# Kernel tuning notes

Hardware: AMD Instinct MI355X
Metric: run time of the kernel (lower is better)

## Reference

```python
import jax, jax.numpy as jnp
import numpy as np

N, M, K, C, OUT = 200000, 50000, 16, 64, 128
EPS = 1e-5  # torch BatchNorm1d default eps


def _bn(h, gamma, beta, mean, var):
    # BatchNorm1d in eval mode (running statistics)
    return (h - mean) * jax.lax.rsqrt(var + EPS) * gamma + beta


def setup_inputs() -> dict:
    key = jax.random.key(0)
    ks = jax.random.split(key, 8)
    p = jax.random.normal(ks[0], (N, 3), jnp.float32)
    x = jax.random.normal(ks[1], (N, C), jnp.float32)
    idx = jax.random.randint(ks[2], (M,), 0, N)          # FPS-sampled center indices
    knn_idx = jax.random.randint(ks[3], (M, K), 0, N)    # KNN neighbor indices
    # channel_shrinker: Linear(3+C, C, bias=False) -> BN -> ReLU -> Linear(C, 1)
    W1 = jax.random.normal(ks[4], (3 + C, C), jnp.float32) * 0.05  # stored [in,out]
    g1 = jnp.ones((C,), jnp.float32); b1 = jnp.zeros((C,), jnp.float32)
    m1 = jnp.zeros((C,), jnp.float32); v1 = jnp.ones((C,), jnp.float32)
    W2 = jax.random.normal(ks[5], (C, 1), jnp.float32) * 0.05
    b2 = jnp.zeros((1,), jnp.float32)
    # linear2: Linear(C, OUT, bias=False) -> BN -> ReLU
    Wl = jax.random.normal(ks[6], (C, OUT), jnp.float32) * 0.05
    gl = jnp.ones((OUT,), jnp.float32); bl = jnp.zeros((OUT,), jnp.float32)
    ml = jnp.zeros((OUT,), jnp.float32); vl = jnp.ones((OUT,), jnp.float32)
    return {"p": p, "x": x, "W1": W1, "g1": g1, "b1": b1, "m1": m1, "v1": v1,
            "W2": W2, "b2": b2, "Wl": Wl, "gl": gl, "bl": bl, "ml": ml, "vl": vl,
            "idx": idx, "knn_idx": knn_idx}


def reference(p, x, W1, g1, b1, m1, v1, W2, b2, Wl, gl, bl, ml, vl, idx, knn_idx):
    # queryandgroup(use_xyz=True): relative xyz of neighbors + gathered features
    n_p = p[idx]                                   # [M,3] sampled centers
    rel = p[knn_idx] - n_p[:, None, :]             # [M,K,3]
    x_knn = jnp.concatenate([rel, x[knn_idx]], -1) # [M,K,3+C]
    # channel_shrinker
    h = jnp.maximum(_bn(x_knn @ W1, g1, b1, m1, v1), 0.0)   # [M,K,C]
    s = h @ W2 + b2                                          # [M,K,1]
    prob = jax.nn.softmax(s, axis=1)                         # softmax over neighbors
    # linear2 on ALL original points, then gather by knn_idx
    y = jnp.maximum(_bn(x @ Wl, gl, bl, ml, vl), 0.0)        # [N,OUT]
    y_knn = y[knn_idx]                                       # [M,K,OUT]
    out = jnp.sum(y_knn * prob, axis=1)                      # [M,OUT]
    return n_p, out
```

## Files before the change

### kernel.cpp

```cpp
#include <hip/hip_runtime.h>

#define EPS 1e-5f

typedef __attribute__((ext_vector_type(8))) short bf16x8;
typedef __attribute__((ext_vector_type(4))) float f32x4;

static __device__ __forceinline__ unsigned short f2bf(float f) {
  unsigned int u = __float_as_uint(f);
  u = u + 0x7FFFu + ((u >> 16) & 1u);
  return (unsigned short)(u >> 16);
}
static __device__ __forceinline__ float bf2f(unsigned short h) {
  return __uint_as_float(((unsigned int)h) << 16);
}
static __device__ __forceinline__ unsigned int pk2(float lo, float hi) {
  return (unsigned int)f2bf(lo) | ((unsigned int)f2bf(hi) << 16);
}

__global__ __launch_bounds__(256) void k1_mfma(
    const float* __restrict__ x, const float* __restrict__ W1,
    const float* __restrict__ Wl, const float* __restrict__ gl,
    const float* __restrict__ bl, const float* __restrict__ ml,
    const float* __restrict__ vl,
    unsigned short* __restrict__ Z, unsigned short* __restrict__ Y)
{
  __shared__ unsigned short As[64 * 64];
  __shared__ unsigned short Bs[192 * 64];
  char* Ab = reinterpret_cast<char*>(As);
  char* Bb = reinterpret_cast<char*>(Bs);

  const int t = threadIdx.x;
  const long row0 = (long)blockIdx.x * 64;

  {
    int k = t >> 2, c0 = (t & 3) * 16;
    const float4* w4 = reinterpret_cast<const float4*>(W1 + (size_t)(3 + k) * 64 + c0);
#pragma unroll
    for (int i = 0; i < 4; ++i) {
      float4 w = w4[i];
#pragma unroll
      for (int j = 0; j < 4; ++j) {
        int c = c0 + i * 4 + j;
        float v = (j == 0) ? w.x : (j == 1) ? w.y : (j == 2) ? w.z : w.w;
        int byte = c * 128 + ((2 * k) ^ ((c & 7) << 4));
        *reinterpret_cast<unsigned short*>(Bb + byte) = f2bf(v);
      }
    }
  }
  {
    int k = t >> 2, c0 = (t & 3) * 32;
    const float4* w4 = reinterpret_cast<const float4*>(Wl + (size_t)k * 128 + c0);
#pragma unroll
    for (int i = 0; i < 8; ++i) {
      float4 w = w4[i];
#pragma unroll
      for (int j = 0; j < 4; ++j) {
        int c = 64 + c0 + i * 4 + j;
        float v = (j == 0) ? w.x : (j == 1) ? w.y : (j == 2) ? w.z : w.w;
        int byte = c * 128 + ((2 * k) ^ ((c & 7) << 4));
        *reinterpret_cast<unsigned short*>(Bb + byte) = f2bf(v);
      }
    }
  }
  {
    const float4* xg = reinterpret_cast<const float4*>(x + row0 * 64);
#pragma unroll
    for (int i = 0; i < 4; ++i) {
      int idx = t + i * 256;
      float4 v = xg[idx];
      int r = idx >> 4;
      int b0 = (idx & 15) * 8;
      int byte = r * 128 + (b0 ^ ((r & 7) << 4));
      uint2 pkv = make_uint2(pk2(v.x, v.y), pk2(v.z, v.w));
      *reinterpret_cast<uint2*>(Ab + byte) = pkv;
    }
  }
  __syncthreads();

  const int wid = t >> 6, lane = t & 63;
  const int roff = (wid & 1) * 32, coff = (wid >> 1) * 96;
  const int lr = lane & 15, lk = lane >> 4;

  bf16x8 af[2][2];
#pragma unroll
  for (int rt = 0; rt < 2; ++rt) {
    int r = roff + rt * 16 + lr;
#pragma unroll
    for (int ks = 0; ks < 2; ++ks) {
      int byte = r * 128 + ((ks * 64 + lk * 16) ^ ((r & 7) << 4));
      af[rt][ks] = *reinterpret_cast<const bf16x8*>(Ab + byte);
    }
  }

#pragma unroll
  for (int ct = 0; ct < 6; ++ct) {
    int c0t = coff + ct * 16;
    int cread = c0t + lr;
    int byte0 = cread * 128 + ((lk * 16) ^ ((cread & 7) << 4));
    int byte1 = cread * 128 + ((64 + lk * 16) ^ ((cread & 7) << 4));
    bf16x8 bf0 = *reinterpret_cast<const bf16x8*>(Bb + byte0);
    bf16x8 bf1 = *reinterpret_cast<const bf16x8*>(Bb + byte1);

    float sc0 = 1.f, sc1 = 1.f, sc2 = 1.f, sc3 = 1.f;
    float sh0 = 0.f, sh1 = 0.f, sh2 = 0.f, sh3 = 0.f;
    if (c0t >= 64) {
      int oc = c0t - 64 + lk * 4;
      float4 g4 = *reinterpret_cast<const float4*>(gl + oc);
      float4 v4 = *reinterpret_cast<const float4*>(vl + oc);
      float4 b4 = *reinterpret_cast<const float4*>(bl + oc);
      float4 m4 = *reinterpret_cast<const float4*>(ml + oc);
      sc0 = g4.x * rsqrtf(v4.x + EPS); sh0 = b4.x - m4.x * sc0;
      sc1 = g4.y * rsqrtf(v4.y + EPS); sh1 = b4.y - m4.y * sc1;
      sc2 = g4.z * rsqrtf(v4.z + EPS); sh2 = b4.z - m4.z * sc2;
      sc3 = g4.w * rsqrtf(v4.w + EPS); sh3 = b4.w - m4.w * sc3;
    }
#pragma unroll
    for (int rt = 0; rt < 2; ++rt) {
      f32x4 acc = {0.f, 0.f, 0.f, 0.f};
      acc = __builtin_amdgcn_mfma_f32_16x16x32_bf16(bf0, af[rt][0], acc, 0, 0, 0);
      acc = __builtin_amdgcn_mfma_f32_16x16x32_bf16(bf1, af[rt][1], acc, 0, 0, 0);
      long n = row0 + roff + rt * 16 + lr;
      if (c0t < 64) {
        int cb = c0t + lk * 4;
        *reinterpret_cast<ushort4*>(Z + n * 64 + cb) =
            make_ushort4(f2bf(acc[0]), f2bf(acc[1]), f2bf(acc[2]), f2bf(acc[3]));
      } else {
        int cb = c0t - 64 + lk * 4;
        float y0 = fmaxf(fmaf(acc[0], sc0, sh0), 0.f);
        float y1 = fmaxf(fmaf(acc[1], sc1, sh1), 0.f);
        float y2 = fmaxf(fmaf(acc[2], sc2, sh2), 0.f);
        float y3 = fmaxf(fmaf(acc[3], sc3, sh3), 0.f);
        *reinterpret_cast<ushort4*>(Y + n * 128 + cb) =
            make_ushort4(f2bf(y0), f2bf(y1), f2bf(y2), f2bf(y3));
      }
    }
  }
}

static __device__ __forceinline__ float comb(float a, float b, int off, int lane) {
  bool hi = (lane & off) != 0;
  float send = hi ? a : b;
  float t = __shfl_xor(send, off, 64);
  return (hi ? b : a) + t;
}

__global__ __launch_bounds__(256) void k2_gather(
    const float* __restrict__ p, const unsigned short* __restrict__ Z,
    const unsigned short* __restrict__ Y, const float* __restrict__ W1,
    const float* __restrict__ g1, const float* __restrict__ b1,
    const float* __restrict__ m1, const float* __restrict__ v1,
    const float* __restrict__ W2, const int* __restrict__ idx,
    const int* __restrict__ knn, float* __restrict__ out_np,
    float* __restrict__ out_feat, int M)
{
  int gtid = blockIdx.x * 256 + threadIdx.x;
  int wid = gtid >> 6;
  int lane = threadIdx.x & 63;
  if (wid >= M) return;
  int m = __builtin_amdgcn_readfirstlane(wid);

  float a1 = g1[lane] * rsqrtf(v1[lane] + EPS);
  float c1 = b1[lane] - m1[lane] * a1;
  float w2 = W2[lane];
  float w10 = W1[lane];
  float w11 = W1[64 + lane];
  float w12 = W1[128 + lane];

  int ic = idx[m];
  float cx = p[ic * 3 + 0];
  float cy = p[ic * 3 + 1];
  float cz = p[ic * 3 + 2];
  if (lane < 3) {
    float v = (lane == 0) ? cx : ((lane == 1) ? cy : cz);
    out_np[(size_t)m * 3 + lane] = v;
  }

  float part[16];
  int jj[16];
#pragma unroll
  for (int k = 0; k < 16; ++k) {
    int j = knn[m * 16 + k];
    jj[k] = j;
    float rx = p[j * 3 + 0] - cx;
    float ry = p[j * 3 + 1] - cy;
    float rz = p[j * 3 + 2] - cz;
    float tv = bf2f(Z[(size_t)j * 64 + lane]);
    tv = fmaf(rx, w10, tv);
    tv = fmaf(ry, w11, tv);
    tv = fmaf(rz, w12, tv);
    float h = fmaxf(fmaf(tv, a1, c1), 0.f);
    part[k] = h * w2;
  }

  float u[8];
#pragma unroll
  for (int i = 0; i < 8; ++i) u[i] = comb(part[2 * i], part[2 * i + 1], 32, lane);
  float v4[4];
#pragma unroll
  for (int i = 0; i < 4; ++i) v4[i] = comb(u[2 * i], u[2 * i + 1], 16, lane);
  float w4[2];
#pragma unroll
  for (int i = 0; i < 2; ++i) w4[i] = comb(v4[2 * i], v4[2 * i + 1], 8, lane);
  float s1 = comb(w4[0], w4[1], 4, lane);
  s1 += __shfl_xor(s1, 1, 64);
  s1 += __shfl_xor(s1, 2, 64);

  float mx = s1;
  mx = fmaxf(mx, __shfl_xor(mx, 4, 64));
  mx = fmaxf(mx, __shfl_xor(mx, 8, 64));
  mx = fmaxf(mx, __shfl_xor(mx, 16, 64));
  mx = fmaxf(mx, __shfl_xor(mx, 32, 64));
  float e = __expf(s1 - mx);

  float pk[16];
  float S = 0.f;
#pragma unroll
  for (int k = 0; k < 16; ++k) {
    int g = ((k & 1) << 3) | ((k & 2) << 1) | ((k & 4) >> 1) | ((k & 8) >> 3);
    pk[k] = __shfl(e, g * 4, 64);
    S += pk[k];
  }
  float inv = 1.f / S;

  float acc0 = 0.f, acc1 = 0.f;
#pragma unroll
  for (int k = 0; k < 16; ++k) {
    const unsigned short* yr = Y + (size_t)jj[k] * 128;
    unsigned int uu = *reinterpret_cast<const unsigned int*>(yr + 2 * lane);
    acc0 = fmaf(pk[k], bf2f((unsigned short)(uu & 0xFFFFu)), acc0);
    acc1 = fmaf(pk[k], bf2f((unsigned short)(uu >> 16)), acc1);
  }
  float* orow = out_feat + (size_t)m * 128;
  *reinterpret_cast<float2*>(orow + 2 * lane) =
      make_float2(acc0 * inv, acc1 * inv);
}

extern "C" void kernel_launch(void* const* d_in, const int* in_sizes, int n_in,
                              void* d_out, int out_size, void* d_ws, size_t ws_size,
                              hipStream_t stream) {
  const float* p  = (const float*)d_in[0];
  const float* x  = (const float*)d_in[1];
  const float* W1 = (const float*)d_in[2];
  const float* g1 = (const float*)d_in[3];
  const float* b1 = (const float*)d_in[4];
  const float* m1 = (const float*)d_in[5];
  const float* v1 = (const float*)d_in[6];
  const float* W2 = (const float*)d_in[7];
  const float* Wl = (const float*)d_in[9];
  const float* gl = (const float*)d_in[10];
  const float* bl = (const float*)d_in[11];
  const float* ml = (const float*)d_in[12];
  const float* vl = (const float*)d_in[13];
  const int* idx  = (const int*)d_in[14];
  const int* knn  = (const int*)d_in[15];

  const int N = in_sizes[1] / 64;
  const int M = in_sizes[14];

  unsigned short* Z = (unsigned short*)d_ws;
  unsigned short* Y = Z + (size_t)N * 64;
  float* out_np   = (float*)d_out;
  float* out_feat = out_np + (size_t)M * 3;

  k1_mfma<<<dim3(N / 64), dim3(256), 0, stream>>>(
      x, W1, Wl, gl, bl, ml, vl, Z, Y);
  k2_gather<<<dim3(((size_t)M * 64 + 255) / 256), dim3(256), 0, stream>>>(
      p, Z, Y, W1, g1, b1, m1, v1, W2, idx, knn, out_np, out_feat, M);
}
```

Baseline: 226.0 us.

## Batch gather loads up front in k2 and widen LDS stores in k1

In the gather kernel, all 16 neighbor indices, point coordinates, Z rows and Y rows are loaded into registers before any compute. This gives many independent outstanding memory requests, so gather latency overlaps instead of being serialized through the softmax dependency chain. In the MFMA kernel, weight and x staging now packs pairs into 16-byte LDS stores instead of per-element 2-byte or 8-byte stores, though the weight global loads become scalar column-strided reads. The cost is higher register pressure in k2, which could lower occupancy.

```diff
diff --git a/kernel.cpp b/kernel.cpp
--- a/kernel.cpp
+++ b/kernel.cpp
@@ -33,46 +33,48 @@
   const long row0 = (long)blockIdx.x * 64;
 
   {
-    int k = t >> 2, c0 = (t & 3) * 16;
-    const float4* w4 = reinterpret_cast<const float4*>(W1 + (size_t)(3 + k) * 64 + c0);
-#pragma unroll
-    for (int i = 0; i < 4; ++i) {
-      float4 w = w4[i];
-#pragma unroll
-      for (int j = 0; j < 4; ++j) {
-        int c = c0 + i * 4 + j;
-        float v = (j == 0) ? w.x : (j == 1) ? w.y : (j == 2) ? w.z : w.w;
-        int byte = c * 128 + ((2 * k) ^ ((c & 7) << 4));
-        *reinterpret_cast<unsigned short*>(Bb + byte) = f2bf(v);
+    int c = t & 63, k0 = (t >> 6) * 16;
+    unsigned int w[8];
+#pragma unroll
+    for (int i = 0; i < 8; ++i) {
+      float lo = W1[(size_t)(3 + k0 + 2 * i) * 64 + c];
+      float hi = W1[(size_t)(3 + k0 + 2 * i + 1) * 64 + c];
+      w[i] = pk2(lo, hi);
+    }
+    int byte0 = c * 128 + ((2 * k0) ^ ((c & 7) << 4));
+    int byte1 = c * 128 + ((2 * (k0 + 8)) ^ ((c & 7) << 4));
+    *reinterpret_cast<uint4*>(Bb + byte0) = make_uint4(w[0], w[1], w[2], w[3]);
+    *reinterpret_cast<uint4*>(Bb + byte1) = make_uint4(w[4], w[5], w[6], w[7]);
+  }
+  {
+    int c = t & 127, kh = t >> 7;
+    int cc = 64 + c;
+#pragma unroll
+    for (int g = 0; g < 4; ++g) {
+      unsigned int w[4];
+#pragma unroll
+      for (int i = 0; i < 4; ++i) {
+        int k = kh * 32 + g * 8 + 2 * i;
+        float lo = Wl[(size_t)k * 128 + c];
+        float hi = Wl[(size_t)(k + 1) * 128 + c];
+        w[i] = pk2(lo, hi);
       }
-    }
-  }
-  {
-    int k = t >> 2, c0 = (t & 3) * 32;
-    const float4* w4 = reinterpret_cast<const float4*>(Wl + (size_t)k * 128 + c0);
-#pragma unroll
-    for (int i = 0; i < 8; ++i) {
-      float4 w = w4[i];
-#pragma unroll
-      for (int j = 0; j < 4; ++j) {
-        int c = 64 + c0 + i * 4 + j;
-        float v = (j == 0) ? w.x : (j == 1) ? w.y : (j == 2) ? w.z : w.w;
-        int byte = c * 128 + ((2 * k) ^ ((c & 7) << 4));
-        *reinterpret_cast<unsigned short*>(Bb + byte) = f2bf(v);
-      }
+      int byte = cc * 128 + ((2 * (kh * 32 + g * 8)) ^ ((cc & 7) << 4));
+      *reinterpret_cast<uint4*>(Bb + byte) = make_uint4(w[0], w[1], w[2], w[3]);
     }
   }
   {
     const float4* xg = reinterpret_cast<const float4*>(x + row0 * 64);
 #pragma unroll
-    for (int i = 0; i < 4; ++i) {
-      int idx = t + i * 256;
-      float4 v = xg[idx];
-      int r = idx >> 4;
-      int b0 = (idx & 15) * 8;
-      int byte = r * 128 + (b0 ^ ((r & 7) << 4));
-      uint2 pkv = make_uint2(pk2(v.x, v.y), pk2(v.z, v.w));
-      *reinterpret_cast<uint2*>(Ab + byte) = pkv;
+    for (int i = 0; i < 2; ++i) {
+      int pi = t + i * 256;
+      int r = pi >> 3, q = pi & 7;
+      float4 v0 = xg[pi * 2];
+      float4 v1 = xg[pi * 2 + 1];
+      int byte = r * 128 + ((q * 16) ^ ((r & 7) << 4));
+      *reinterpret_cast<uint4*>(Ab + byte) =
+          make_uint4(pk2(v0.x, v0.y), pk2(v0.z, v0.w),
+                     pk2(v1.x, v1.y), pk2(v1.z, v1.w));
     }
   }
   __syncthreads();
@@ -159,6 +161,32 @@
   if (wid >= M) return;
   int m = __builtin_amdgcn_readfirstlane(wid);
 
+  int ic = idx[m];
+  float cx = p[ic * 3 + 0];
+  float cy = p[ic * 3 + 1];
+  float cz = p[ic * 3 + 2];
+
+  int jj[16];
+#pragma unroll
+  for (int k = 0; k < 16; ++k) jj[k] = knn[m * 16 + k];
+
+  float px[16], py[16], pz[16];
+#pragma unroll
+  for (int k = 0; k < 16; ++k) {
+    px[k] = p[jj[k] * 3 + 0];
+    py[k] = p[jj[k] * 3 + 1];
+    pz[k] = p[jj[k] * 3 + 2];
+  }
+
+  unsigned short zv[16];
+#pragma unroll
+  for (int k = 0; k < 16; ++k) zv[k] = Z[(size_t)jj[k] * 64 + lane];
+
+  unsigned int yv[16];
+#pragma unroll
+  for (int k = 0; k < 16; ++k)
+    yv[k] = *reinterpret_cast<const unsigned int*>(Y + (size_t)jj[k] * 128 + 2 * lane);
+
   float a1 = g1[lane] * rsqrtf(v1[lane] + EPS);
   float c1 = b1[lane] - m1[lane] * a1;
   float w2 = W2[lane];
@@ -166,28 +194,18 @@
   float w11 = W1[64 + lane];
   float w12 = W1[128 + lane];
 
-  int ic = idx[m];
-  float cx = p[ic * 3 + 0];
-  float cy = p[ic * 3 + 1];
-  float cz = p[ic * 3 + 2];
   if (lane < 3) {
     float v = (lane == 0) ? cx : ((lane == 1) ? cy : cz);
     out_np[(size_t)m * 3 + lane] = v;
   }
 
   float part[16];
-  int jj[16];
-#pragma unroll
-  for (int k = 0; k < 16; ++k) {
-    int j = knn[m * 16 + k];
-    jj[k] = j;
-    float rx = p[j * 3 + 0] - cx;
-    float ry = p[j * 3 + 1] - cy;
-    float rz = p[j * 3 + 2] - cz;
-    float tv = bf2f(Z[(size_t)j * 64 + lane]);
-    tv = fmaf(rx, w10, tv);
-    tv = fmaf(ry, w11, tv);
-    tv = fmaf(rz, w12, tv);
+#pragma unroll
+  for (int k = 0; k < 16; ++k) {
+    float tv = bf2f(zv[k]);
+    tv = fmaf(px[k] - cx, w10, tv);
+    tv = fmaf(py[k] - cy, w11, tv);
+    tv = fmaf(pz[k] - cz, w12, tv);
     float h = fmaxf(fmaf(tv, a1, c1), 0.f);
     part[k] = h * w2;
   }
@@ -212,23 +230,21 @@
   mx = fmaxf(mx, __shfl_xor(mx, 32, 64));
   float e = __expf(s1 - mx);
 
-  float pk[16];
+  float pw[16];
   float S = 0.f;
 #pragma unroll
   for (int k = 0; k < 16; ++k) {
     int g = ((k & 1) << 3) | ((k & 2) << 1) | ((k & 4) >> 1) | ((k & 8) >> 3);
-    pk[k] = __shfl(e, g * 4, 64);
-    S += pk[k];
+    pw[k] = __shfl(e, g * 4, 64);
+    S += pw[k];
   }
   float inv = 1.f / S;
 
   float acc0 = 0.f, acc1 = 0.f;
 #pragma unroll
   for (int k = 0; k < 16; ++k) {
-    const unsigned short* yr = Y + (size_t)jj[k] * 128;
-    unsigned int uu = *reinterpret_cast<const unsigned int*>(yr + 2 * lane);
-    acc0 = fmaf(pk[k], bf2f((unsigned short)(uu & 0xFFFFu)), acc0);
-    acc1 = fmaf(pk[k], bf2f((unsigned short)(uu >> 16)), acc1);
+    acc0 = fmaf(pw[k], bf2f((unsigned short)(yv[k] & 0xFFFFu)), acc0);
+    acc1 = fmaf(pw[k], bf2f((unsigned short)(yv[k] >> 16)), acc1);
   }
   float* orow = out_feat + (size_t)m * 128;
   *reinterpret_cast<float2*>(orow + 2 * lane) =
```

Measured after the change: 205.3 us. 1.1x faster.
